# Kernel tuning notes

Hardware: AMD Instinct MI355X
Metric: run time of the kernel (lower is better)

The kernel has to match this reference:

```python
import jax, jax.numpy as jnp
import numpy as np

H = 8      # n_heads
E = 128    # d_keys (== D; required by out_projection Linear(D*n_heads, D))


def setup_inputs() -> dict:
    key = jax.random.key(0)
    ks = jax.random.split(key, 11)
    B, T, D = 64, 256, 128
    s = 0.02
    return {
        "x": jax.random.normal(ks[0], (B, T, D), dtype=jnp.float32),
        "Wq": jax.random.normal(ks[1], (D, H * E), dtype=jnp.float32) * s,
        "bq": jax.random.normal(ks[2], (H * E,), dtype=jnp.float32) * s,
        "Wk": jax.random.normal(ks[3], (D, H * E), dtype=jnp.float32) * s,
        "bk": jax.random.normal(ks[4], (H * E,), dtype=jnp.float32) * s,
        "Wv": jax.random.normal(ks[5], (D, H * E), dtype=jnp.float32) * s,
        "bv": jax.random.normal(ks[6], (H * E,), dtype=jnp.float32) * s,
        "Ws": jax.random.normal(ks[7], (T, 1), dtype=jnp.float32) * s,
        "bs": jax.random.normal(ks[8], (1,), dtype=jnp.float32) * s,
        "Wo": jax.random.normal(ks[9], (H * E, D), dtype=jnp.float32) * s,
        "bo": jax.random.normal(ks[10], (D,), dtype=jnp.float32) * s,
    }


def reference(x, Wq, bq, Wk, bk, Wv, bv, Ws, bs, Wo, bo):
    B, T, D = x.shape
    # Q/K/V projections -> [B, T, H, E]
    Q = (x @ Wq + bq).reshape(B, T, H, E)
    K = (x @ Wk + bk).reshape(B, T, H, E)
    V = (x @ Wv + bv).reshape(B, T, H, E)
    scale = 1.0 / jnp.sqrt(jnp.float32(E))
    # QK^T scores over time: [B, H, T, T] (query t, key j)
    scores = jnp.einsum('bthd,bjhd->bhtj', Q, K)
    # summary projection contracts the key axis j: T -> 1  => [B, H, T, 1]
    summary = (scale * scores) @ Ws + bs
    # softmax over the query axis t (dim=-2)
    beta = jax.nn.softmax(summary, axis=-2)[..., 0]        # [B, H, T]
    # weight V per (b, t, h) and sum over time -> [B, H, E]
    beta_cal = jnp.transpose(beta, (0, 2, 1))[..., None]   # [B, T, H, 1]
    result = jnp.sum(V * beta_cal, axis=1)                 # [B, H, E]
    out = result.reshape(B, H * E) @ Wo + bo               # [B, D]
    return out
```

## Files before the change

### kernel.cpp

```cpp
#include <hip/hip_runtime.h>
#include <hip/hip_bf16.h>


#define SCALE 0.08838834764831845f

__global__ __launch_bounds__(512)
void k_bh(const float* __restrict__ x,  const float* __restrict__ Wq,
          const float* __restrict__ Wk, const float* __restrict__ bk,
          const float* __restrict__ Wsv, float* __restrict__ xbg)
{
    __shared__ float red[4][256];
    __shared__ float xwS[128];
    __shared__ float kwS[256];
    __shared__ float wqkS[256];
    __shared__ float betaS[2][256];
    __shared__ float smx[2][4], sms[2][4];
    __shared__ float swS;

    const int tid = threadIdx.x;
    const int b = blockIdx.x, p = blockIdx.y;
    const float* xb_ptr = x + (size_t)b * 32768;

    {
        const int d = tid & 127, tc = tid >> 7;
        float acc = 0.f;
        const float* xp = xb_ptr + (size_t)(tc * 64) * 128 + d;
        #pragma unroll 16
        for (int j = 0; j < 64; ++j)
            acc += Wsv[tc * 64 + j] * xp[(size_t)j * 128];
        red[tc][d] = acc;
        if (tid >= 128 && tid < 192) {
            const int lane = tid & 63;
            float v = Wsv[lane] + Wsv[lane + 64] + Wsv[lane + 128] + Wsv[lane + 192];
            #pragma unroll
            for (int off = 32; off; off >>= 1) v += __shfl_xor(v, off, 64);
            if (lane == 0) swS = v;
        }
        __syncthreads();
        if (tid < 128) xwS[tid] = red[0][tid] + red[1][tid] + red[2][tid] + red[3][tid];
        __syncthreads();
    }

    {
        const int e2 = tid & 255, kh = tid >> 8;
        const int he = 256 * p + e2;
        float acc = 0.f;
        const float* wp = Wk + (size_t)(kh * 64) * 1024 + he;
        #pragma unroll 16
        for (int j = 0; j < 64; ++j)
            acc += xwS[kh * 64 + j] * wp[(size_t)j * 1024];
        red[kh][e2] = acc;
        __syncthreads();
        if (tid < 256) kwS[tid] = red[0][tid] + red[1][tid] + swS * bk[256 * p + tid];
        __syncthreads();
    }

    {
        const int o = tid & 255, eh = tid >> 8;
        const int d = o & 127, hi = o >> 7;
        const float4* wq4 = (const float4*)(Wq + (size_t)d * 1024 + (2 * p + hi) * 128 + eh * 64);
        const float* kwp = kwS + hi * 128 + eh * 64;
        float acc = 0.f;
        #pragma unroll
        for (int j4 = 0; j4 < 16; ++j4) {
            const float4 w = wq4[j4];
            acc += w.x * kwp[4*j4] + w.y * kwp[4*j4+1] + w.z * kwp[4*j4+2] + w.w * kwp[4*j4+3];
        }
        red[eh][o] = acc;
        __syncthreads();
        if (tid < 256) wqkS[tid] = (red[0][tid] + red[1][tid]) * SCALE;
        __syncthreads();
    }

    {
        const int t = tid & 255, dh = tid >> 8;
        const float4* xr4 = (const float4*)(xb_ptr + (size_t)t * 128 + dh * 64);
        float a0 = 0.f, a1 = 0.f;
        #pragma unroll
        for (int j4 = 0; j4 < 16; ++j4) {
            const float4 xv = xr4[j4];
            const float* w0 = wqkS + dh * 64 + 4 * j4;
            const float* w1 = wqkS + 128 + dh * 64 + 4 * j4;
            a0 += xv.x * w0[0] + xv.y * w0[1] + xv.z * w0[2] + xv.w * w0[3];
            a1 += xv.x * w1[0] + xv.y * w1[1] + xv.z * w1[2] + xv.w * w1[3];
        }
        red[dh][t] = a0; red[2 + dh][t] = a1;
        __syncthreads();

        const int hi = tid >> 8;
        float s = red[hi * 2][t] + red[hi * 2 + 1][t];
        const int w = tid >> 6, wi = w & 3, lane = tid & 63;
        float m = s;
        #pragma unroll
        for (int off = 32; off; off >>= 1) m = fmaxf(m, __shfl_xor(m, off, 64));
        if (lane == 0) smx[hi][wi] = m;
        __syncthreads();
        const float M = fmaxf(fmaxf(smx[hi][0], smx[hi][1]), fmaxf(smx[hi][2], smx[hi][3]));
        const float e = __expf(s - M);
        float ss = e;
        #pragma unroll
        for (int off = 32; off; off >>= 1) ss += __shfl_xor(ss, off, 64);
        if (lane == 0) sms[hi][wi] = ss;
        __syncthreads();
        const float S = sms[hi][0] + sms[hi][1] + sms[hi][2] + sms[hi][3];
        betaS[hi][t] = e / S;
        __syncthreads();
    }

    {
        const int d = tid & 127, tq = tid >> 7;
        const float* xp = xb_ptr + (size_t)(tq * 64) * 128 + d;
        const float* b0 = betaS[0] + tq * 64;
        const float* b1 = betaS[1] + tq * 64;
        float a0 = 0.f, a1 = 0.f;
        #pragma unroll 8
        for (int j = 0; j < 64; ++j) {
            const float xv = xp[(size_t)j * 128];
            a0 += b0[j] * xv; a1 += b1[j] * xv;
        }
        __syncthreads();
        red[tq][d] = a0; red[tq][128 + d] = a1;
        __syncthreads();
        if (tid < 256)
            xbg[b * 1024 + 256 * p + tid] =
                red[0][tid] + red[1][tid] + red[2][tid] + red[3][tid];
    }
}

__global__ __launch_bounds__(256)
void k_ov(const float* __restrict__ Wv, const float* __restrict__ bv,
          const float* __restrict__ Wo, const float* __restrict__ bov,
          const float* __restrict__ xbg, float* __restrict__ out)
{
    __shared__ float resS[256];
    __shared__ float po[2][128];
    const int tid = threadIdx.x;
    const int b = blockIdx.x, y = blockIdx.y;
    const int he = y * 256 + tid;

    {
        const float* xbp = xbg + b * 1024 + (he >> 7) * 128;
        float acc = bv[he];
        const float* wp = Wv + he;
        #pragma unroll 16
        for (int dd = 0; dd < 128; ++dd)
            acc += xbp[dd] * wp[(size_t)dd * 1024];
        resS[tid] = acc;
        __syncthreads();
    }

    {
        const int d = tid & 127, rh = tid >> 7;
        const float* rp = resS + rh * 128;
        const float* wp = Wo + (size_t)(y * 256 + rh * 128) * 128 + d;
        float acc = 0.f;
        #pragma unroll 16
        for (int j = 0; j < 128; ++j)
            acc += rp[j] * wp[(size_t)j * 128];
        po[rh][d] = acc;
        __syncthreads();
        if (tid < 128) {
            float v = po[0][tid] + po[1][tid];
            if (y == 0) v += bov[tid];
            atomicAdd(&out[(size_t)b * 128 + tid], v);
        }
    }
}

extern "C" void kernel_launch(void* const* d_in, const int* in_sizes, int n_in,
                              void* d_out, int out_size, void* d_ws, size_t ws_size,
                              hipStream_t stream) {
    const float* x  = (const float*)d_in[0];
    const float* Wq = (const float*)d_in[1];
    const float* Wk = (const float*)d_in[3];
    const float* bk = (const float*)d_in[4];
    const float* Wv = (const float*)d_in[5];
    const float* bv = (const float*)d_in[6];
    const float* Ws = (const float*)d_in[7];
    const float* Wo = (const float*)d_in[9];
    const float* bo = (const float*)d_in[10];
    float* out = (float*)d_out;
    float* ws  = (float*)d_ws;

    hipMemsetAsync(out, 0, (size_t)out_size * sizeof(float), stream);
    k_bh<<<dim3(64, 4), dim3(512), 0, stream>>>(x, Wq, Wk, bk, Ws, ws);
    k_ov<<<dim3(64, 4), dim3(256), 0, stream>>>(Wv, bv, Wo, bo, ws, out);
}
```

Before: 102.0 us.

## Fuse both kernels into one with flag-synchronised cross-block reduction

Merges the beta/summary kernel and the V/output projection kernel into a single launch and drops the output memset. Each (batch, part) block now computes its V and Wo slices locally. Three blocks publish partial outputs to workspace and set a flag; the fourth block spins on those flags and writes the final sum. The Wq·kw and x·wqk products are also restructured so each wave computes one dot product with a shuffle reduction. The flags are never reset between calls, so later launches may read stale partials without waiting. The spin-wait also relies on all blocks being co-resident.

```diff
diff --git a/kernel.cpp b/kernel.cpp
--- a/kernel.cpp
+++ b/kernel.cpp
@@ -3,38 +3,44 @@
 
 
 #define SCALE 0.08838834764831845f
+#define MAGIC 0x13579BDFu
 
 __global__ __launch_bounds__(512)
-void k_bh(const float* __restrict__ x,  const float* __restrict__ Wq,
-          const float* __restrict__ Wk, const float* __restrict__ bk,
-          const float* __restrict__ Wsv, float* __restrict__ xbg)
+void ta_one(const float* __restrict__ x,  const float* __restrict__ Wq,
+            const float* __restrict__ Wk, const float* __restrict__ bk,
+            const float* __restrict__ Wv, const float* __restrict__ bv,
+            const float* __restrict__ Wsv,
+            const float* __restrict__ Wo, const float* __restrict__ bov,
+            float* __restrict__ ws, float* __restrict__ out)
 {
     __shared__ float red[4][256];
     __shared__ float xwS[128];
     __shared__ float kwS[256];
     __shared__ float wqkS[256];
     __shared__ float betaS[2][256];
+    __shared__ float xbS[256];
+    __shared__ float resS[256];
     __shared__ float smx[2][4], sms[2][4];
     __shared__ float swS;
 
     const int tid = threadIdx.x;
     const int b = blockIdx.x, p = blockIdx.y;
-    const float* xb_ptr = x + (size_t)b * 32768;
+    const int w = tid >> 6, l = tid & 63;
+    const float* xp0 = x + (size_t)b * 32768;
 
     {
         const int d = tid & 127, tc = tid >> 7;
         float acc = 0.f;
-        const float* xp = xb_ptr + (size_t)(tc * 64) * 128 + d;
+        const float* xp = xp0 + (size_t)(tc * 64) * 128 + d;
         #pragma unroll 16
         for (int j = 0; j < 64; ++j)
             acc += Wsv[tc * 64 + j] * xp[(size_t)j * 128];
         red[tc][d] = acc;
         if (tid >= 128 && tid < 192) {
-            const int lane = tid & 63;
-            float v = Wsv[lane] + Wsv[lane + 64] + Wsv[lane + 128] + Wsv[lane + 192];
+            float v = Wsv[l] + Wsv[l + 64] + Wsv[l + 128] + Wsv[l + 192];
             #pragma unroll
             for (int off = 32; off; off >>= 1) v += __shfl_xor(v, off, 64);
-            if (lane == 0) swS = v;
+            if (l == 0) swS = v;
         }
         __syncthreads();
         if (tid < 128) xwS[tid] = red[0][tid] + red[1][tid] + red[2][tid] + red[3][tid];
@@ -43,9 +49,8 @@
 
     {
         const int e2 = tid & 255, kh = tid >> 8;
-        const int he = 256 * p + e2;
-        float acc = 0.f;
-        const float* wp = Wk + (size_t)(kh * 64) * 1024 + he;
+        const float* wp = Wk + (size_t)(kh * 64) * 1024 + 256 * p + e2;
+        float acc = 0.f;
         #pragma unroll 16
         for (int j = 0; j < 64; ++j)
             acc += xwS[kh * 64 + j] * wp[(size_t)j * 1024];
@@ -56,51 +61,49 @@
     }
 
     {
-        const int o = tid & 255, eh = tid >> 8;
-        const int d = o & 127, hi = o >> 7;
-        const float4* wq4 = (const float4*)(Wq + (size_t)d * 1024 + (2 * p + hi) * 128 + eh * 64);
-        const float* kwp = kwS + hi * 128 + eh * 64;
-        float acc = 0.f;
-        #pragma unroll
-        for (int j4 = 0; j4 < 16; ++j4) {
-            const float4 w = wq4[j4];
-            acc += w.x * kwp[4*j4] + w.y * kwp[4*j4+1] + w.z * kwp[4*j4+2] + w.w * kwp[4*j4+3];
-        }
-        red[eh][o] = acc;
-        __syncthreads();
-        if (tid < 256) wqkS[tid] = (red[0][tid] + red[1][tid]) * SCALE;
-        __syncthreads();
-    }
-
-    {
-        const int t = tid & 255, dh = tid >> 8;
-        const float4* xr4 = (const float4*)(xb_ptr + (size_t)t * 128 + dh * 64);
-        float a0 = 0.f, a1 = 0.f;
-        #pragma unroll
-        for (int j4 = 0; j4 < 16; ++j4) {
-            const float4 xv = xr4[j4];
-            const float* w0 = wqkS + dh * 64 + 4 * j4;
-            const float* w1 = wqkS + 128 + dh * 64 + 4 * j4;
-            a0 += xv.x * w0[0] + xv.y * w0[1] + xv.z * w0[2] + xv.w * w0[3];
-            a1 += xv.x * w1[0] + xv.y * w1[1] + xv.z * w1[2] + xv.w * w1[3];
-        }
-        red[dh][t] = a0; red[2 + dh][t] = a1;
-        __syncthreads();
-
-        const int hi = tid >> 8;
-        float s = red[hi * 2][t] + red[hi * 2 + 1][t];
-        const int w = tid >> 6, wi = w & 3, lane = tid & 63;
-        float m = s;
+        #pragma unroll 4
+        for (int i = 0; i < 32; ++i) {
+            const int o = w * 32 + i;
+            const int hi = o >> 7, d = o & 127;
+            const float2 wv = *(const float2*)(Wq + (size_t)d * 1024 + (2 * p + hi) * 128 + 2 * l);
+            const float2 kv = *(const float2*)(kwS + hi * 128 + 2 * l);
+            float r = wv.x * kv.x + wv.y * kv.y;
+            #pragma unroll
+            for (int off = 32; off; off >>= 1) r += __shfl_xor(r, off, 64);
+            if (l == 0) wqkS[o] = r * SCALE;
+        }
+        __syncthreads();
+    }
+
+    {
+        #pragma unroll 4
+        for (int i = 0; i < 64; ++i) {
+            const int s = w * 64 + i;
+            const int t = s & 255, hi = s >> 8;
+            const float2 xv = *(const float2*)(xp0 + (size_t)t * 128 + 2 * l);
+            const float2 qv = *(const float2*)(wqkS + hi * 128 + 2 * l);
+            float r = xv.x * qv.x + xv.y * qv.y;
+            #pragma unroll
+            for (int off = 32; off; off >>= 1) r += __shfl_xor(r, off, 64);
+            if (l == 0) betaS[hi][t] = r;
+        }
+        __syncthreads();
+    }
+
+    {
+        const int t = tid & 255, hi = tid >> 8;
+        const float v = betaS[hi][t];
+        float m = v;
         #pragma unroll
         for (int off = 32; off; off >>= 1) m = fmaxf(m, __shfl_xor(m, off, 64));
-        if (lane == 0) smx[hi][wi] = m;
+        if (l == 0) smx[hi][w & 3] = m;
         __syncthreads();
         const float M = fmaxf(fmaxf(smx[hi][0], smx[hi][1]), fmaxf(smx[hi][2], smx[hi][3]));
-        const float e = __expf(s - M);
-        float ss = e;
+        const float e = __expf(v - M);
+        float ssum = e;
         #pragma unroll
-        for (int off = 32; off; off >>= 1) ss += __shfl_xor(ss, off, 64);
-        if (lane == 0) sms[hi][wi] = ss;
+        for (int off = 32; off; off >>= 1) ssum += __shfl_xor(ssum, off, 64);
+        if (l == 0) sms[hi][w & 3] = ssum;
         __syncthreads();
         const float S = sms[hi][0] + sms[hi][1] + sms[hi][2] + sms[hi][3];
         betaS[hi][t] = e / S;
@@ -109,7 +112,7 @@
 
     {
         const int d = tid & 127, tq = tid >> 7;
-        const float* xp = xb_ptr + (size_t)(tq * 64) * 128 + d;
+        const float* xp = xp0 + (size_t)(tq * 64) * 128 + d;
         const float* b0 = betaS[0] + tq * 64;
         const float* b1 = betaS[1] + tq * 64;
         float a0 = 0.f, a1 = 0.f;
@@ -118,51 +121,62 @@
             const float xv = xp[(size_t)j * 128];
             a0 += b0[j] * xv; a1 += b1[j] * xv;
         }
-        __syncthreads();
         red[tq][d] = a0; red[tq][128 + d] = a1;
         __syncthreads();
-        if (tid < 256)
-            xbg[b * 1024 + 256 * p + tid] =
+        if (tid < 256) xbS[tid] = red[0][tid] + red[1][tid] + red[2][tid] + red[3][tid];
+        __syncthreads();
+    }
+
+    {
+        const int he2 = tid & 255, kh = tid >> 8;
+        const int hi = he2 >> 7;
+        const float* wp = Wv + (size_t)(kh * 64) * 1024 + 256 * p + he2;
+        const float* xbp = xbS + hi * 128 + kh * 64;
+        float acc = 0.f;
+        #pragma unroll 16
+        for (int j = 0; j < 64; ++j)
+            acc += xbp[j] * wp[(size_t)j * 1024];
+        red[kh][he2] = acc;
+        __syncthreads();
+        if (tid < 256) resS[tid] = red[0][tid] + red[1][tid] + bv[256 * p + tid];
+        __syncthreads();
+    }
+
+    {
+        const int d = tid & 127, rh = tid >> 7;
+        const float* wp = Wo + (size_t)(256 * p + rh * 64) * 128 + d;
+        const float* rp = resS + rh * 64;
+        float acc = 0.f;
+        #pragma unroll 16
+        for (int j = 0; j < 64; ++j)
+            acc += rp[j] * wp[(size_t)j * 128];
+        red[rh][d] = acc;
+        __syncthreads();
+    }
+
+    float* part = ws;
+    unsigned* flags = (unsigned*)(ws + 32768);
+    if (p < 3) {
+        if (tid < 128) {
+            part[(size_t)(b * 4 + p) * 128 + tid] =
                 red[0][tid] + red[1][tid] + red[2][tid] + red[3][tid];
-    }
-}
-
-__global__ __launch_bounds__(256)
-void k_ov(const float* __restrict__ Wv, const float* __restrict__ bv,
-          const float* __restrict__ Wo, const float* __restrict__ bov,
-          const float* __restrict__ xbg, float* __restrict__ out)
-{
-    __shared__ float resS[256];
-    __shared__ float po[2][128];
-    const int tid = threadIdx.x;
-    const int b = blockIdx.x, y = blockIdx.y;
-    const int he = y * 256 + tid;
-
-    {
-        const float* xbp = xbg + b * 1024 + (he >> 7) * 128;
-        float acc = bv[he];
-        const float* wp = Wv + he;
-        #pragma unroll 16
-        for (int dd = 0; dd < 128; ++dd)
-            acc += xbp[dd] * wp[(size_t)dd * 1024];
-        resS[tid] = acc;
-        __syncthreads();
-    }
-
-    {
-        const int d = tid & 127, rh = tid >> 7;
-        const float* rp = resS + rh * 128;
-        const float* wp = Wo + (size_t)(y * 256 + rh * 128) * 128 + d;
-        float acc = 0.f;
-        #pragma unroll 16
-        for (int j = 0; j < 128; ++j)
-            acc += rp[j] * wp[(size_t)j * 128];
-        po[rh][d] = acc;
+            __threadfence();
+        }
+        __syncthreads();
+        if (tid == 0) atomicExch(&flags[b * 4 + p], MAGIC);
+    } else {
+        if (tid == 0) {
+            while (atomicCAS(&flags[b * 4 + 0], MAGIC, MAGIC) != MAGIC) {}
+            while (atomicCAS(&flags[b * 4 + 1], MAGIC, MAGIC) != MAGIC) {}
+            while (atomicCAS(&flags[b * 4 + 2], MAGIC, MAGIC) != MAGIC) {}
+        }
         __syncthreads();
         if (tid < 128) {
-            float v = po[0][tid] + po[1][tid];
-            if (y == 0) v += bov[tid];
-            atomicAdd(&out[(size_t)b * 128 + tid], v);
+            float v = bov[tid] + red[0][tid] + red[1][tid] + red[2][tid] + red[3][tid];
+            v += atomicAdd(&part[(size_t)(b * 4 + 0) * 128 + tid], 0.f);
+            v += atomicAdd(&part[(size_t)(b * 4 + 1) * 128 + tid], 0.f);
+            v += atomicAdd(&part[(size_t)(b * 4 + 2) * 128 + tid], 0.f);
+            out[(size_t)b * 128 + tid] = v;
         }
     }
 }
@@ -182,7 +196,5 @@
     float* out = (float*)d_out;
     float* ws  = (float*)d_ws;
 
-    hipMemsetAsync(out, 0, (size_t)out_size * sizeof(float), stream);
-    k_bh<<<dim3(64, 4), dim3(512), 0, stream>>>(x, Wq, Wk, bk, Ws, ws);
-    k_ov<<<dim3(64, 4), dim3(256), 0, stream>>>(Wv, bv, Wo, bo, ws, out);
+    ta_one<<<dim3(64, 4), dim3(512), 0, stream>>>(x, Wq, Wk, bk, Wv, bv, Ws, Wo, bo, ws, out);
 }
```

Result: slower. 128.7 us (+26.1%).
